# Optimization experiments

Hardware: AMD Instinct MI355X
Metric: run time of the kernel (lower is better)

## Reference

```python
import jax, jax.numpy as jnp
import numpy as np

D_MODEL = 512
D_ATTN = 512

def setup_inputs() -> dict:
    key = jax.random.key(0)
    kx, kq, kk, kv = jax.random.split(key, 4)
    x = jax.random.normal(kx, (8, 2048, D_MODEL), dtype=jnp.float32)
    s = 1.0 / np.sqrt(D_MODEL)
    Wq = jax.random.normal(kq, (D_ATTN, D_MODEL), dtype=jnp.float32) * s
    Wk = jax.random.normal(kk, (D_ATTN, D_MODEL), dtype=jnp.float32) * s
    Wv = jax.random.normal(kv, (D_MODEL, D_MODEL), dtype=jnp.float32) * s
    return {"x": x, "Wq": Wq, "Wk": Wk, "Wv": Wv}

def reference(x, Wq, Wk, Wv):
    # x: [B, S, D]; Linear(bias=False): y = x @ W.T
    q = jnp.einsum('bsd,ad->bsa', x, Wq)  # [B,S,Da]
    k = jnp.einsum('bsd,ad->bsa', x, Wk)  # [B,S,Da]
    v = jnp.einsum('bsd,ed->bse', x, Wv)  # [B,S,Dv]
    scale = 1.0 / jnp.sqrt(jnp.asarray(q.shape[-1], dtype=q.dtype))
    scores = jnp.einsum('bqa,bka->bqk', q, k) * scale  # [B,S,S]
    p = jax.nn.softmax(scores, axis=-1)
    return jnp.einsum('bqk,bke->bqe', p, v)
```

## Files before the change

kernel.cpp:

```cpp
#include <hip/hip_runtime.h>


typedef __bf16 bf16x8 __attribute__((ext_vector_type(8)));
typedef __bf16 bf16x4 __attribute__((ext_vector_type(4)));
typedef float  f32x4  __attribute__((ext_vector_type(4)));

constexpr int SEQ = 2048;
constexpr int DM  = 512;
constexpr int NB  = 8;
constexpr int GS  = NB * SEQ;
constexpr int NT2 = SEQ / 32;

__device__ __forceinline__ void gl16(const void* g, void* l) {
  __builtin_amdgcn_global_load_lds((const __attribute__((address_space(1))) void*)g,
                                   (__attribute__((address_space(3))) void*)l, 16, 0, 0);
}

__device__ __forceinline__ f32x4 mfma16(bf16x8 a, bf16x8 b, f32x4 c) {
  return __builtin_amdgcn_mfma_f32_16x16x32_bf16(a, b, c, 0, 0, 0);
}

__global__ void convert_kernel(const float* __restrict__ x,
                               const float* __restrict__ wq,
                               const float* __restrict__ wk,
                               const float* __restrict__ wv,
                               __bf16* __restrict__ xb,
                               __bf16* __restrict__ wqb,
                               __bf16* __restrict__ wkb,
                               __bf16* __restrict__ wvb) {
  const int NX4 = (GS * DM) / 4;
  const int NW4 = (DM * DM) / 4;
  const int stride = gridDim.x * blockDim.x;
  const int tid = blockIdx.x * blockDim.x + threadIdx.x;
  for (int i = tid; i < NX4; i += stride) {
    float4 v = ((const float4*)x)[i];
    bf16x4 o = { (__bf16)v.x, (__bf16)v.y, (__bf16)v.z, (__bf16)v.w };
    ((bf16x4*)xb)[i] = o;
  }
  for (int i = tid; i < NW4; i += stride) {
    float4 v = ((const float4*)wq)[i];
    bf16x4 o = { (__bf16)v.x, (__bf16)v.y, (__bf16)v.z, (__bf16)v.w };
    ((bf16x4*)wqb)[i] = o;
  }
  for (int i = tid; i < NW4; i += stride) {
    float4 v = ((const float4*)wk)[i];
    bf16x4 o = { (__bf16)v.x, (__bf16)v.y, (__bf16)v.z, (__bf16)v.w };
    ((bf16x4*)wkb)[i] = o;
  }
  for (int i = tid; i < NW4; i += stride) {
    float4 v = ((const float4*)wv)[i];
    bf16x4 o = { (__bf16)v.x, (__bf16)v.y, (__bf16)v.z, (__bf16)v.w };
    ((bf16x4*)wvb)[i] = o;
  }
}

__global__ __launch_bounds__(256, 2) void gemm_nt_kernel(
    const __bf16* __restrict__ A, const __bf16* __restrict__ Bm,
    __bf16* __restrict__ C, int N) {
  __shared__ __bf16 As[128 * 32];
  __shared__ __bf16 Bs[128 * 32];
  const int t = threadIdx.x;
  const int w = t >> 6, l = t & 63;
  const int l15 = l & 15, lg = l >> 4;
  const int m0 = blockIdx.x * 128, n0 = blockIdx.y * 128;
  const int wr = w >> 1, wc = w & 1;

  f32x4 acc[4][4] = {};
  const char* Ab = (const char*)A + (size_t)m0 * (DM * 2);
  const char* Bb = (const char*)Bm + (size_t)n0 * (DM * 2);

  for (int k0 = 0; k0 < DM; k0 += 32) {
#pragma unroll
    for (int i = 0; i < 2; ++i) {
      const int f = (i * 256 + t) * 16;
      const int row = f >> 6, c = f & 63;
      gl16(Ab + (size_t)row * (DM * 2) + k0 * 2 + c, (char*)As + f);
      gl16(Bb + (size_t)row * (DM * 2) + k0 * 2 + c, (char*)Bs + f);
    }
    __syncthreads();
    bf16x8 af[4], bfr[4];
#pragma unroll
    for (int mi = 0; mi < 4; ++mi)
      af[mi] = *(const bf16x8*)((const char*)As + (wr * 64 + mi * 16 + l15) * 64 + lg * 16);
#pragma unroll
    for (int ni = 0; ni < 4; ++ni)
      bfr[ni] = *(const bf16x8*)((const char*)Bs + (wc * 64 + ni * 16 + l15) * 64 + lg * 16);
#pragma unroll
    for (int mi = 0; mi < 4; ++mi)
#pragma unroll
      for (int ni = 0; ni < 4; ++ni)
        acc[mi][ni] = mfma16(af[mi], bfr[ni], acc[mi][ni]);
    __syncthreads();
  }
#pragma unroll
  for (int mi = 0; mi < 4; ++mi)
#pragma unroll
    for (int ni = 0; ni < 4; ++ni)
#pragma unroll
      for (int r = 0; r < 4; ++r) {
        const int row = m0 + wr * 64 + mi * 16 + lg * 4 + r;
        const int col = n0 + wc * 64 + ni * 16 + l15;
        C[(size_t)row * N + col] = (__bf16)acc[mi][ni][r];
      }
}

__global__ __launch_bounds__(256, 2) void attn_kernel(
    const __bf16* __restrict__ QK, const __bf16* __restrict__ Vt,
    float* __restrict__ Out) {
  __shared__ __bf16 Ks[32 * 512];
  __shared__ __bf16 Vs[512 * 32];
  __shared__ float  Ss[32 * 36];
  __shared__ __bf16 Ps[32 * 32];
  __shared__ float  m_s[32], l_s[32], corr_s[32];
  __shared__ int    flags_s[4];

  const int t = threadIdx.x;
  const int w = t >> 6, l = t & 63;
  const int l15 = l & 15, lg = l >> 4;
  const int bid = blockIdx.x;
  const int b = bid & 7;
  const int q0 = (bid >> 3) * 32;
  const int qi = w >> 1, kj = w & 1;

  bf16x8 qf[16];
  {
    const char* Qb = (const char*)QK +
        (size_t)(b * SEQ + q0 + qi * 16 + l15) * 2048 + lg * 16;
#pragma unroll
    for (int ks = 0; ks < 16; ++ks)
      qf[ks] = *(const bf16x8*)(Qb + ks * 64);
  }

  f32x4 o[2][8] = {};
  if (t < 32) { m_s[t] = -__builtin_inff(); l_s[t] = 0.f; }

  const char* Kb = (const char*)QK + (size_t)b * SEQ * 2048 + 1024;
  const char* Vb = (const char*)Vt + (size_t)b * SEQ * 2;

#pragma unroll
  for (int i = 0; i < 8; ++i) {
    const int f = (i * 256 + t) * 16;
    const int row = f >> 10, c = f & 1023;
    gl16(Kb + (size_t)row * 2048 + (c ^ ((row & 7) << 4)), (char*)Ks + f);
  }
  __syncthreads();

  const float SCL = 0.0637639022f;

  for (int it = 0; it < NT2; ++it) {
    const int kv0 = it * 32;

#pragma unroll
    for (int i = 0; i < 8; ++i) {
      const int f = (i * 256 + t) * 16;
      const int e = f >> 6, c2 = f & 63;
      gl16(Vb + (size_t)e * (GS * 2) + (size_t)kv0 * 2 + (c2 ^ ((e & 3) << 4)),
           (char*)Vs + f);
    }
    {
      f32x4 sa = {};
      const int krow = kj * 16 + l15;
      const char* KsR = (const char*)Ks + krow * 1024;
      const int ksw = (krow & 7) << 4;
#pragma unroll
      for (int ks = 0; ks < 16; ++ks) {
        bf16x8 kf = *(const bf16x8*)(KsR + ((ks * 64 + lg * 16) ^ ksw));
        sa = mfma16(qf[ks], kf, sa);
      }
#pragma unroll
      for (int r = 0; r < 4; ++r)
        Ss[(qi * 16 + lg * 4 + r) * 36 + kj * 16 + l15] = sa[r] * SCL;
    }
    __syncthreads();

    {
      const int row = t >> 3, c8 = t & 7;
      float4 v0 = *(const float4*)&Ss[row * 36 + c8 * 4];
      float tmax = fmaxf(fmaxf(v0.x, v0.y), fmaxf(v0.z, v0.w));
      tmax = fmaxf(tmax, __shfl_xor(tmax, 1));
      tmax = fmaxf(tmax, __shfl_xor(tmax, 2));
      tmax = fmaxf(tmax, __shfl_xor(tmax, 4));
      const float mold = m_s[row];
      const float mnew = fmaxf(mold, tmax);
      const float corr = exp2f(mold - mnew);
      const float p0 = exp2f(v0.x - mnew), p1 = exp2f(v0.y - mnew);
      const float p2 = exp2f(v0.z - mnew), p3 = exp2f(v0.w - mnew);
      float rsum = (p0 + p1) + (p2 + p3);
      rsum += __shfl_xor(rsum, 1);
      rsum += __shfl_xor(rsum, 2);
      rsum += __shfl_xor(rsum, 4);
      if (c8 == 0) { m_s[row] = mnew; l_s[row] = l_s[row] * corr + rsum; corr_s[row] = corr; }
      const int allskip = __all(corr == 1.0f);
      if (l == 0) flags_s[w] = allskip;
      bf16x4 pb = { (__bf16)p0, (__bf16)p1, (__bf16)p2, (__bf16)p3 };
      *(bf16x4*)((char*)Ps + row * 64 + (((c8 >> 1) * 16) ^ ((row & 3) << 4)) +
                 (c8 & 1) * 8) = pb;
    }
    __syncthreads();

    {
      const int kvn = ((it + 1) == NT2 ? 0 : (it + 1)) * 32;
#pragma unroll
      for (int i = 0; i < 8; ++i) {
        const int f = (i * 256 + t) * 16;
        const int row = f >> 10, c = f & 1023;
        gl16(Kb + (size_t)(kvn + row) * 2048 + (c ^ ((row & 7) << 4)), (char*)Ks + f);
      }
      const int fl = flags_s[0] & flags_s[1] & flags_s[2] & flags_s[3];
      if (!fl) {
#pragma unroll
        for (int mi = 0; mi < 2; ++mi) {
          float cr[4];
#pragma unroll
          for (int r = 0; r < 4; ++r) cr[r] = corr_s[mi * 16 + lg * 4 + r];
#pragma unroll
          for (int ni = 0; ni < 8; ++ni)
#pragma unroll
            for (int r = 0; r < 4; ++r) o[mi][ni][r] *= cr[r];
        }
      }
      bf16x8 pf[2];
#pragma unroll
      for (int mi = 0; mi < 2; ++mi) {
        const int prow = mi * 16 + l15;
        pf[mi] = *(const bf16x8*)((const char*)Ps + prow * 64 +
                                  ((lg * 16) ^ ((prow & 3) << 4)));
      }
#pragma unroll
      for (int ni = 0; ni < 8; ++ni) {
        const int er = w * 128 + ni * 16 + l15;
        bf16x8 vf = *(const bf16x8*)((const char*)Vs + er * 64 +
                                     ((lg * 16) ^ ((er & 3) << 4)));
#pragma unroll
        for (int mi = 0; mi < 2; ++mi)
          o[mi][ni] = mfma16(pf[mi], vf, o[mi][ni]);
      }
    }
    __syncthreads();
  }

#pragma unroll
  for (int mi = 0; mi < 2; ++mi) {
    float rl[4];
#pragma unroll
    for (int r = 0; r < 4; ++r) rl[r] = 1.0f / l_s[mi * 16 + lg * 4 + r];
#pragma unroll
    for (int ni = 0; ni < 8; ++ni)
#pragma unroll
      for (int r = 0; r < 4; ++r) {
        const int row = q0 + mi * 16 + lg * 4 + r;
        const int col = w * 128 + ni * 16 + l15;
        Out[((size_t)b * SEQ + row) * DM + col] = o[mi][ni][r] * rl[r];
      }
  }
}

extern "C" void kernel_launch(void* const* d_in, const int* in_sizes, int n_in,
                              void* d_out, int out_size, void* d_ws, size_t ws_size,
                              hipStream_t stream) {
  const float* x  = (const float*)d_in[0];
  const float* wq = (const float*)d_in[1];
  const float* wk = (const float*)d_in[2];
  const float* wv = (const float*)d_in[3];
  float* out = (float*)d_out;
  char* ws = (char*)d_ws;

  __bf16* xb   = (__bf16*)(ws);
  __bf16* wqkb = (__bf16*)(ws + 16777216);
  __bf16* wvb  = (__bf16*)(ws + 17825792);
  __bf16* qk   = (__bf16*)(ws + 18350080);
  __bf16* vt   = (__bf16*)(ws + 51904512);

  convert_kernel<<<2048, 256, 0, stream>>>(x, wq, wk, wv,
                                           xb, wqkb, wqkb + 262144, wvb);
  gemm_nt_kernel<<<dim3(GS / 128, 1024 / 128), 256, 0, stream>>>(xb, wqkb, qk, 1024);
  gemm_nt_kernel<<<dim3(DM / 128, GS / 128), 256, 0, stream>>>(wvb, xb, vt, GS);
  attn_kernel<<<512, 256, 0, stream>>>(qk, vt, out);
}
```

Baseline: 273.3 us.

## Double-buffer K/V tiles and widen attention blocks to 64 query rows

```diff
diff --git a/kernel.cpp b/kernel.cpp
--- a/kernel.cpp
+++ b/kernel.cpp
@@ -104,23 +104,36 @@
       }
 }
 
-__global__ __launch_bounds__(256, 2) void attn_kernel(
+__global__ __launch_bounds__(512, 2) void attn_kernel(
     const __bf16* __restrict__ QK, const __bf16* __restrict__ Vt,
     float* __restrict__ Out) {
-  __shared__ __bf16 Ks[32 * 512];
-  __shared__ __bf16 Vs[512 * 32];
-  __shared__ float  Ss[32 * 36];
-  __shared__ __bf16 Ps[32 * 32];
-  __shared__ float  m_s[32], l_s[32], corr_s[32];
-  __shared__ int    flags_s[4];
+  __shared__ __bf16 Ks[2][32 * 512];
+  __shared__ __bf16 Vs[2][512 * 32];
+  __shared__ float  Ss[64 * 36];
+  __shared__ __bf16 Ps[64 * 32];
+  __shared__ float  m_s[64], l_s[64], corr_s[64];
+  __shared__ int    flags_s[8];
 
   const int t = threadIdx.x;
   const int w = t >> 6, l = t & 63;
   const int l15 = l & 15, lg = l >> 4;
-  const int bid = blockIdx.x;
-  const int b = bid & 7;
-  const int q0 = (bid >> 3) * 32;
+  const int b = blockIdx.x & 7;
+  const int q0 = (blockIdx.x >> 3) * 64;
   const int qi = w >> 1, kj = w & 1;
+
+  int ksrc[4], vsrc[4], ldst[4];
+#pragma unroll
+  for (int i = 0; i < 4; ++i) {
+    const int f = (i * 512 + t) * 16;
+    ldst[i] = f;
+    const int krow = f >> 10, kc = f & 1023;
+    ksrc[i] = krow * 2048 + (kc ^ ((krow & 7) << 4));
+    const int e = f >> 6, c2 = f & 63;
+    vsrc[i] = e * (GS * 2) + (c2 ^ ((e & 3) << 4));
+  }
+
+  const char* Kb = (const char*)QK + (size_t)b * SEQ * 2048 + 1024;
+  const char* Vb = (const char*)Vt + (size_t)b * SEQ * 2;
 
   bf16x8 qf[16];
   {
@@ -131,47 +144,53 @@
       qf[ks] = *(const bf16x8*)(Qb + ks * 64);
   }
 
-  f32x4 o[2][8] = {};
-  if (t < 32) { m_s[t] = -__builtin_inff(); l_s[t] = 0.f; }
-
-  const char* Kb = (const char*)QK + (size_t)b * SEQ * 2048 + 1024;
-  const char* Vb = (const char*)Vt + (size_t)b * SEQ * 2;
-
-#pragma unroll
-  for (int i = 0; i < 8; ++i) {
-    const int f = (i * 256 + t) * 16;
-    const int row = f >> 10, c = f & 1023;
-    gl16(Kb + (size_t)row * 2048 + (c ^ ((row & 7) << 4)), (char*)Ks + f);
-  }
-  __syncthreads();
+  f32x4 o[4][4] = {};
+  if (t < 64) { m_s[t] = -__builtin_inff(); l_s[t] = 0.f; }
+
+#pragma unroll
+  for (int i = 0; i < 4; ++i) gl16(Kb + ksrc[i], (char*)&Ks[0][0] + ldst[i]);
+#pragma unroll
+  for (int i = 0; i < 4; ++i) gl16(Vb + vsrc[i], (char*)&Vs[0][0] + ldst[i]);
 
   const float SCL = 0.0637639022f;
 
   for (int it = 0; it < NT2; ++it) {
-    const int kv0 = it * 32;
-
-#pragma unroll
-    for (int i = 0; i < 8; ++i) {
-      const int f = (i * 256 + t) * 16;
-      const int e = f >> 6, c2 = f & 63;
-      gl16(Vb + (size_t)e * (GS * 2) + (size_t)kv0 * 2 + (c2 ^ ((e & 3) << 4)),
-           (char*)Vs + f);
-    }
-    {
-      f32x4 sa = {};
+    const int cur = it & 1;
+
+    asm volatile("s_waitcnt vmcnt(0) lgkmcnt(0)" ::: "memory");
+    __builtin_amdgcn_s_barrier();
+
+    {
+      const int kvn = (it + 1 < NT2 ? it + 1 : 0) * 32;
+      char* kdst = (char*)&Ks[cur ^ 1][0];
+      char* vdst = (char*)&Vs[cur ^ 1][0];
+#pragma unroll
+      for (int i = 0; i < 4; ++i) gl16(Kb + (size_t)kvn * 2048 + ksrc[i], kdst + ldst[i]);
+#pragma unroll
+      for (int i = 0; i < 4; ++i) gl16(Vb + (size_t)kvn * 2 + vsrc[i], vdst + ldst[i]);
+    }
+
+    {
+      f32x4 s0 = {}, s1 = {};
       const int krow = kj * 16 + l15;
-      const char* KsR = (const char*)Ks + krow * 1024;
+      const char* KsR = (const char*)&Ks[cur][0] + krow * 1024;
       const int ksw = (krow & 7) << 4;
-#pragma unroll
-      for (int ks = 0; ks < 16; ++ks) {
-        bf16x8 kf = *(const bf16x8*)(KsR + ((ks * 64 + lg * 16) ^ ksw));
-        sa = mfma16(qf[ks], kf, sa);
-      }
+      __builtin_amdgcn_s_setprio(1);
+#pragma unroll
+      for (int ks = 0; ks < 8; ++ks) {
+        bf16x8 kf0 = *(const bf16x8*)(KsR + ((ks * 64 + lg * 16) ^ ksw));
+        bf16x8 kf1 = *(const bf16x8*)(KsR + (((ks + 8) * 64 + lg * 16) ^ ksw));
+        s0 = mfma16(qf[ks], kf0, s0);
+        s1 = mfma16(qf[ks + 8], kf1, s1);
+      }
+      __builtin_amdgcn_s_setprio(0);
+      s0 = s0 + s1;
 #pragma unroll
       for (int r = 0; r < 4; ++r)
-        Ss[(qi * 16 + lg * 4 + r) * 36 + kj * 16 + l15] = sa[r] * SCL;
-    }
-    __syncthreads();
+        Ss[(qi * 16 + lg * 4 + r) * 36 + kj * 16 + l15] = s0[r] * SCL;
+    }
+    asm volatile("s_waitcnt lgkmcnt(0)" ::: "memory");
+    __builtin_amdgcn_s_barrier();
 
     {
       const int row = t >> 3, c8 = t & 7;
@@ -196,60 +215,57 @@
       *(bf16x4*)((char*)Ps + row * 64 + (((c8 >> 1) * 16) ^ ((row & 3) << 4)) +
                  (c8 & 1) * 8) = pb;
     }
-    __syncthreads();
-
-    {
-      const int kvn = ((it + 1) == NT2 ? 0 : (it + 1)) * 32;
-#pragma unroll
-      for (int i = 0; i < 8; ++i) {
-        const int f = (i * 256 + t) * 16;
-        const int row = f >> 10, c = f & 1023;
-        gl16(Kb + (size_t)(kvn + row) * 2048 + (c ^ ((row & 7) << 4)), (char*)Ks + f);
-      }
-      const int fl = flags_s[0] & flags_s[1] & flags_s[2] & flags_s[3];
+    asm volatile("s_waitcnt lgkmcnt(0)" ::: "memory");
+    __builtin_amdgcn_s_barrier();
+
+    {
+      int fl = 1;
+#pragma unroll
+      for (int i = 0; i < 8; ++i) fl &= flags_s[i];
       if (!fl) {
 #pragma unroll
-        for (int mi = 0; mi < 2; ++mi) {
+        for (int mi = 0; mi < 4; ++mi) {
           float cr[4];
 #pragma unroll
           for (int r = 0; r < 4; ++r) cr[r] = corr_s[mi * 16 + lg * 4 + r];
 #pragma unroll
-          for (int ni = 0; ni < 8; ++ni)
+          for (int ni = 0; ni < 4; ++ni)
 #pragma unroll
             for (int r = 0; r < 4; ++r) o[mi][ni][r] *= cr[r];
         }
       }
-      bf16x8 pf[2];
-#pragma unroll
-      for (int mi = 0; mi < 2; ++mi) {
+      bf16x8 pf[4];
+#pragma unroll
+      for (int mi = 0; mi < 4; ++mi) {
         const int prow = mi * 16 + l15;
         pf[mi] = *(const bf16x8*)((const char*)Ps + prow * 64 +
                                   ((lg * 16) ^ ((prow & 3) << 4)));
       }
-#pragma unroll
-      for (int ni = 0; ni < 8; ++ni) {
-        const int er = w * 128 + ni * 16 + l15;
-        bf16x8 vf = *(const bf16x8*)((const char*)Vs + er * 64 +
+      __builtin_amdgcn_s_setprio(1);
+#pragma unroll
+      for (int ni = 0; ni < 4; ++ni) {
+        const int er = w * 64 + ni * 16 + l15;
+        bf16x8 vf = *(const bf16x8*)((const char*)&Vs[cur][0] + er * 64 +
                                      ((lg * 16) ^ ((er & 3) << 4)));
 #pragma unroll
-        for (int mi = 0; mi < 2; ++mi)
+        for (int mi = 0; mi < 4; ++mi)
           o[mi][ni] = mfma16(pf[mi], vf, o[mi][ni]);
       }
-    }
-    __syncthreads();
-  }
-
-#pragma unroll
-  for (int mi = 0; mi < 2; ++mi) {
+      __builtin_amdgcn_s_setprio(0);
+    }
+  }
+
+#pragma unroll
+  for (int mi = 0; mi < 4; ++mi) {
     float rl[4];
 #pragma unroll
     for (int r = 0; r < 4; ++r) rl[r] = 1.0f / l_s[mi * 16 + lg * 4 + r];
 #pragma unroll
-    for (int ni = 0; ni < 8; ++ni)
+    for (int ni = 0; ni < 4; ++ni)
 #pragma unroll
       for (int r = 0; r < 4; ++r) {
         const int row = q0 + mi * 16 + lg * 4 + r;
-        const int col = w * 128 + ni * 16 + l15;
+        const int col = w * 64 + ni * 16 + l15;
         Out[((size_t)b * SEQ + row) * DM + col] = o[mi][ni][r] * rl[r];
       }
   }
@@ -275,5 +291,5 @@
                                            xb, wqkb, wqkb + 262144, wvb);
   gemm_nt_kernel<<<dim3(GS / 128, 1024 / 128), 256, 0, stream>>>(xb, wqkb, qk, 1024);
   gemm_nt_kernel<<<dim3(DM / 128, GS / 128), 256, 0, stream>>>(wvb, xb, vt, GS);
-  attn_kernel<<<512, 256, 0, stream>>>(qk, vt, out);
-}
+  attn_kernel<<<256, 512, 0, stream>>>(qk, vt, out);
+}
```

New measurement: 289.6 us. +6.0%, slower.

## Split attention QK^T across 8 waves with LDS atomic reduction and fold scale into Wq

Applied to the files above, without the earlier changes.

```diff
diff --git a/kernel.cpp b/kernel.cpp
--- a/kernel.cpp
+++ b/kernel.cpp
@@ -30,6 +30,7 @@
                                __bf16* __restrict__ wvb) {
   const int NX4 = (GS * DM) / 4;
   const int NW4 = (DM * DM) / 4;
+  const float SCL = 0.0637639022f;
   const int stride = gridDim.x * blockDim.x;
   const int tid = blockIdx.x * blockDim.x + threadIdx.x;
   for (int i = tid; i < NX4; i += stride) {
@@ -39,7 +40,8 @@
   }
   for (int i = tid; i < NW4; i += stride) {
     float4 v = ((const float4*)wq)[i];
-    bf16x4 o = { (__bf16)v.x, (__bf16)v.y, (__bf16)v.z, (__bf16)v.w };
+    bf16x4 o = { (__bf16)(v.x * SCL), (__bf16)(v.y * SCL),
+                 (__bf16)(v.z * SCL), (__bf16)(v.w * SCL) };
     ((bf16x4*)wqb)[i] = o;
   }
   for (int i = tid; i < NW4; i += stride) {
@@ -104,109 +106,123 @@
       }
 }
 
-__global__ __launch_bounds__(256, 2) void attn_kernel(
+__global__ __launch_bounds__(512, 4) void attn_kernel(
     const __bf16* __restrict__ QK, const __bf16* __restrict__ Vt,
     float* __restrict__ Out) {
-  __shared__ __bf16 Ks[32 * 512];
-  __shared__ __bf16 Vs[512 * 32];
-  __shared__ float  Ss[32 * 36];
+  __shared__ __align__(16) __bf16 Ks[32 * 512];
+  __shared__ __align__(16) __bf16 Vs[512 * 32];
+  __shared__ float  Sa[32 * 34];
   __shared__ __bf16 Ps[32 * 32];
   __shared__ float  m_s[32], l_s[32], corr_s[32];
-  __shared__ int    flags_s[4];
+  __shared__ int    flags_s[8];
 
   const int t = threadIdx.x;
   const int w = t >> 6, l = t & 63;
   const int l15 = l & 15, lg = l >> 4;
-  const int bid = blockIdx.x;
-  const int b = bid & 7;
-  const int q0 = (bid >> 3) * 32;
-  const int qi = w >> 1, kj = w & 1;
-
-  bf16x8 qf[16];
-  {
-    const char* Qb = (const char*)QK +
-        (size_t)(b * SEQ + q0 + qi * 16 + l15) * 2048 + lg * 16;
-#pragma unroll
-    for (int ks = 0; ks < 16; ++ks)
-      qf[ks] = *(const bf16x8*)(Qb + ks * 64);
-  }
-
-  f32x4 o[2][8] = {};
-  if (t < 32) { m_s[t] = -__builtin_inff(); l_s[t] = 0.f; }
-
+  const int b = blockIdx.x & 7;
+  const int q0 = (blockIdx.x >> 3) * 32;
+  const int dh = w & 3;
+  const int kj = w >> 2;
+
+  char* KsB = (char*)Ks;
+  char* VsB = (char*)Vs;
   const char* Kb = (const char*)QK + (size_t)b * SEQ * 2048 + 1024;
   const char* Vb = (const char*)Vt + (size_t)b * SEQ * 2;
 
-#pragma unroll
-  for (int i = 0; i < 8; ++i) {
-    const int f = (i * 256 + t) * 16;
-    const int row = f >> 10, c = f & 1023;
-    gl16(Kb + (size_t)row * 2048 + (c ^ ((row & 7) << 4)), (char*)Ks + f);
-  }
+  const int krow_sw = (w & 7) << 4;
+  const int ksrc0 = w * 2048 + ((l * 16) ^ krow_sw);
+  const int ve = t >> 2;
+  const int vsrc0 = (((t & 3) << 4) ^ ((ve & 3) << 4));
+  const int vdst0 = ve * 64 + ((t & 3) << 4);
+
+  bf16x8 qf[2][4];
+  {
+    const char* Qp = (const char*)QK + (size_t)(b * SEQ + q0 + l15) * 2048 +
+                     dh * 256 + lg * 16;
+#pragma unroll
+    for (int mi = 0; mi < 2; ++mi)
+#pragma unroll
+      for (int ks = 0; ks < 4; ++ks)
+        qf[mi][ks] = *(const bf16x8*)(Qp + (size_t)mi * 16 * 2048 + ks * 64);
+  }
+
+  f32x4 o[2][4] = {};
+
+  for (int idx = t; idx < 32 * 34; idx += 512) Sa[idx] = 0.f;
+  if (t < 32) { m_s[t] = -__builtin_inff(); l_s[t] = 0.f; }
+#pragma unroll
+  for (int i = 0; i < 4; ++i)
+    gl16(Kb + i * 8 * 2048 + ksrc0, KsB + (i * 512 + t) * 16);
   __syncthreads();
 
-  const float SCL = 0.0637639022f;
-
   for (int it = 0; it < NT2; ++it) {
-    const int kv0 = it * 32;
-
-#pragma unroll
-    for (int i = 0; i < 8; ++i) {
-      const int f = (i * 256 + t) * 16;
-      const int e = f >> 6, c2 = f & 63;
-      gl16(Vb + (size_t)e * (GS * 2) + (size_t)kv0 * 2 + (c2 ^ ((e & 3) << 4)),
-           (char*)Vs + f);
-    }
+    const size_t kv0 = (size_t)it * 32;
+
+#pragma unroll
+    for (int i = 0; i < 4; ++i)
+      gl16(Vb + kv0 * 2 + (size_t)(i * 128 + ve) * (GS * 2) + vsrc0,
+           VsB + i * 8192 + vdst0);
     {
-      f32x4 sa = {};
-      const int krow = kj * 16 + l15;
-      const char* KsR = (const char*)Ks + krow * 1024;
-      const int ksw = (krow & 7) << 4;
-#pragma unroll
-      for (int ks = 0; ks < 16; ++ks) {
-        bf16x8 kf = *(const bf16x8*)(KsR + ((ks * 64 + lg * 16) ^ ksw));
-        sa = mfma16(qf[ks], kf, sa);
-      }
-#pragma unroll
-      for (int r = 0; r < 4; ++r)
-        Ss[(qi * 16 + lg * 4 + r) * 36 + kj * 16 + l15] = sa[r] * SCL;
+      f32x4 s0 = {}, s1 = {};
+      const char* KsR = KsB + (kj * 16 + l15) * 1024;
+      const int ksw = (l15 & 7) << 4;
+      __builtin_amdgcn_s_setprio(1);
+#pragma unroll
+      for (int ks = 0; ks < 4; ++ks) {
+        bf16x8 kf = *(const bf16x8*)(KsR + ((dh * 256 + ks * 64 + lg * 16) ^ ksw));
+        s0 = mfma16(qf[0][ks], kf, s0);
+        s1 = mfma16(qf[1][ks], kf, s1);
+      }
+      __builtin_amdgcn_s_setprio(0);
+      const int scol = kj * 16 + l15;
+#pragma unroll
+      for (int r = 0; r < 4; ++r) {
+        atomicAdd(&Sa[(lg * 4 + r) * 34 + scol], s0[r]);
+        atomicAdd(&Sa[(16 + lg * 4 + r) * 34 + scol], s1[r]);
+      }
     }
     __syncthreads();
 
     {
-      const int row = t >> 3, c8 = t & 7;
-      float4 v0 = *(const float4*)&Ss[row * 36 + c8 * 4];
-      float tmax = fmaxf(fmaxf(v0.x, v0.y), fmaxf(v0.z, v0.w));
+      const int row = t >> 4, c = t & 15;
+      float a0 = Sa[row * 34 + 2 * c];
+      float a1 = Sa[row * 34 + 2 * c + 1];
+      Sa[row * 34 + 2 * c] = 0.f;
+      Sa[row * 34 + 2 * c + 1] = 0.f;
+      float tmax = fmaxf(a0, a1);
       tmax = fmaxf(tmax, __shfl_xor(tmax, 1));
       tmax = fmaxf(tmax, __shfl_xor(tmax, 2));
       tmax = fmaxf(tmax, __shfl_xor(tmax, 4));
+      tmax = fmaxf(tmax, __shfl_xor(tmax, 8));
       const float mold = m_s[row];
       const float mnew = fmaxf(mold, tmax);
       const float corr = exp2f(mold - mnew);
-      const float p0 = exp2f(v0.x - mnew), p1 = exp2f(v0.y - mnew);
-      const float p2 = exp2f(v0.z - mnew), p3 = exp2f(v0.w - mnew);
-      float rsum = (p0 + p1) + (p2 + p3);
+      const float p0 = exp2f(a0 - mnew), p1 = exp2f(a1 - mnew);
+      float rsum = p0 + p1;
       rsum += __shfl_xor(rsum, 1);
       rsum += __shfl_xor(rsum, 2);
       rsum += __shfl_xor(rsum, 4);
-      if (c8 == 0) { m_s[row] = mnew; l_s[row] = l_s[row] * corr + rsum; corr_s[row] = corr; }
+      rsum += __shfl_xor(rsum, 8);
+      if (c == 0) { m_s[row] = mnew; l_s[row] = l_s[row] * corr + rsum; corr_s[row] = corr; }
       const int allskip = __all(corr == 1.0f);
       if (l == 0) flags_s[w] = allskip;
-      bf16x4 pb = { (__bf16)p0, (__bf16)p1, (__bf16)p2, (__bf16)p3 };
-      *(bf16x4*)((char*)Ps + row * 64 + (((c8 >> 1) * 16) ^ ((row & 3) << 4)) +
-                 (c8 & 1) * 8) = pb;
+      unsigned short u0 = __builtin_bit_cast(unsigned short, (__bf16)p0);
+      unsigned short u1 = __builtin_bit_cast(unsigned short, (__bf16)p1);
+      unsigned int pp = (unsigned int)u0 | ((unsigned int)u1 << 16);
+      *(unsigned int*)((char*)Ps + row * 64 + (((c >> 2) ^ (row & 3)) << 4) +
+                       (c & 3) * 4) = pp;
     }
     __syncthreads();
 
     {
-      const int kvn = ((it + 1) == NT2 ? 0 : (it + 1)) * 32;
-#pragma unroll
-      for (int i = 0; i < 8; ++i) {
-        const int f = (i * 256 + t) * 16;
-        const int row = f >> 10, c = f & 1023;
-        gl16(Kb + (size_t)(kvn + row) * 2048 + (c ^ ((row & 7) << 4)), (char*)Ks + f);
-      }
-      const int fl = flags_s[0] & flags_s[1] & flags_s[2] & flags_s[3];
+      const size_t kvn = (size_t)((it + 1) & (NT2 - 1)) * 32;
+#pragma unroll
+      for (int i = 0; i < 4; ++i)
+        gl16(Kb + (kvn + i * 8) * 2048 + ksrc0, KsB + (i * 512 + t) * 16);
+
+      int fl = 1;
+#pragma unroll
+      for (int i = 0; i < 8; ++i) fl &= flags_s[i];
       if (!fl) {
 #pragma unroll
         for (int mi = 0; mi < 2; ++mi) {
@@ -214,7 +230,7 @@
 #pragma unroll
           for (int r = 0; r < 4; ++r) cr[r] = corr_s[mi * 16 + lg * 4 + r];
 #pragma unroll
-          for (int ni = 0; ni < 8; ++ni)
+          for (int ni = 0; ni < 4; ++ni)
 #pragma unroll
             for (int r = 0; r < 4; ++r) o[mi][ni][r] *= cr[r];
         }
@@ -224,17 +240,19 @@
       for (int mi = 0; mi < 2; ++mi) {
         const int prow = mi * 16 + l15;
         pf[mi] = *(const bf16x8*)((const char*)Ps + prow * 64 +
-                                  ((lg * 16) ^ ((prow & 3) << 4)));
-      }
-#pragma unroll
-      for (int ni = 0; ni < 8; ++ni) {
-        const int er = w * 128 + ni * 16 + l15;
+                                  ((lg ^ (prow & 3)) << 4));
+      }
+      __builtin_amdgcn_s_setprio(1);
+#pragma unroll
+      for (int ni = 0; ni < 4; ++ni) {
+        const int er = w * 64 + ni * 16 + l15;
         bf16x8 vf = *(const bf16x8*)((const char*)Vs + er * 64 +
-                                     ((lg * 16) ^ ((er & 3) << 4)));
+                                     ((lg ^ (er & 3)) << 4));
 #pragma unroll
         for (int mi = 0; mi < 2; ++mi)
           o[mi][ni] = mfma16(pf[mi], vf, o[mi][ni]);
       }
+      __builtin_amdgcn_s_setprio(0);
     }
     __syncthreads();
   }
@@ -245,11 +263,11 @@
 #pragma unroll
     for (int r = 0; r < 4; ++r) rl[r] = 1.0f / l_s[mi * 16 + lg * 4 + r];
 #pragma unroll
-    for (int ni = 0; ni < 8; ++ni)
+    for (int ni = 0; ni < 4; ++ni)
 #pragma unroll
       for (int r = 0; r < 4; ++r) {
         const int row = q0 + mi * 16 + lg * 4 + r;
-        const int col = w * 128 + ni * 16 + l15;
+        const int col = w * 64 + ni * 16 + l15;
         Out[((size_t)b * SEQ + row) * DM + col] = o[mi][ni][r] * rl[r];
       }
   }
@@ -275,5 +293,5 @@
                                            xb, wqkb, wqkb + 262144, wvb);
   gemm_nt_kernel<<<dim3(GS / 128, 1024 / 128), 256, 0, stream>>>(xb, wqkb, qk, 1024);
   gemm_nt_kernel<<<dim3(DM / 128, GS / 128), 256, 0, stream>>>(wvb, xb, vt, GS);
-  attn_kernel<<<512, 256, 0, stream>>>(qk, vt, out);
-}
+  attn_kernel<<<512, 512, 0, stream>>>(qk, vt, out);
+}
```

Result: slower. 926.7 us (+239.1%).

## Double attention KV tile to 64 and stream V fragments straight from global

Applied to the files above, without the earlier changes.

```diff
diff --git a/kernel.cpp b/kernel.cpp
--- a/kernel.cpp
+++ b/kernel.cpp
@@ -9,7 +9,7 @@
 constexpr int DM  = 512;
 constexpr int NB  = 8;
 constexpr int GS  = NB * SEQ;
-constexpr int NT2 = SEQ / 32;
+constexpr int NT  = SEQ / 64;
 
 __device__ __forceinline__ void gl16(const void* g, void* l) {
   __builtin_amdgcn_global_load_lds((const __attribute__((address_space(1))) void*)g,
@@ -30,6 +30,7 @@
                                __bf16* __restrict__ wvb) {
   const int NX4 = (GS * DM) / 4;
   const int NW4 = (DM * DM) / 4;
+  const float SCL = 0.0637639022f;
   const int stride = gridDim.x * blockDim.x;
   const int tid = blockIdx.x * blockDim.x + threadIdx.x;
   for (int i = tid; i < NX4; i += stride) {
@@ -39,7 +40,8 @@
   }
   for (int i = tid; i < NW4; i += stride) {
     float4 v = ((const float4*)wq)[i];
-    bf16x4 o = { (__bf16)v.x, (__bf16)v.y, (__bf16)v.z, (__bf16)v.w };
+    bf16x4 o = { (__bf16)(v.x * SCL), (__bf16)(v.y * SCL),
+                 (__bf16)(v.z * SCL), (__bf16)(v.w * SCL) };
     ((bf16x4*)wqb)[i] = o;
   }
   for (int i = tid; i < NW4; i += stride) {
@@ -107,76 +109,92 @@
 __global__ __launch_bounds__(256, 2) void attn_kernel(
     const __bf16* __restrict__ QK, const __bf16* __restrict__ Vt,
     float* __restrict__ Out) {
-  __shared__ __bf16 Ks[32 * 512];
-  __shared__ __bf16 Vs[512 * 32];
-  __shared__ float  Ss[32 * 36];
-  __shared__ __bf16 Ps[32 * 32];
+  __shared__ __align__(16) __bf16 Ks[64 * 512];
+  __shared__ float  Ss[32 * 68];
+  __shared__ __align__(16) __bf16 Ps[32 * 64];
   __shared__ float  m_s[32], l_s[32], corr_s[32];
   __shared__ int    flags_s[4];
 
   const int t = threadIdx.x;
   const int w = t >> 6, l = t & 63;
   const int l15 = l & 15, lg = l >> 4;
-  const int bid = blockIdx.x;
-  const int b = bid & 7;
-  const int q0 = (bid >> 3) * 32;
+  const int b = blockIdx.x & 7;
+  const int q0 = (blockIdx.x >> 3) * 32;
   const int qi = w >> 1, kj = w & 1;
+
+  char* KsB = (char*)Ks;
+  const char* Kb = (const char*)QK + (size_t)b * SEQ * 2048 + 1024;
+  const char* Vb = (const char*)Vt + (size_t)b * SEQ * 2;
 
   bf16x8 qf[16];
   {
-    const char* Qb = (const char*)QK +
-        (size_t)(b * SEQ + q0 + qi * 16 + l15) * 2048 + lg * 16;
+    const char* Qp = (const char*)QK + (size_t)(b * SEQ + q0 + qi * 16 + l15) * 2048 + lg * 16;
 #pragma unroll
     for (int ks = 0; ks < 16; ++ks)
-      qf[ks] = *(const bf16x8*)(Qb + ks * 64);
+      qf[ks] = *(const bf16x8*)(Qp + ks * 64);
   }
 
   f32x4 o[2][8] = {};
   if (t < 32) { m_s[t] = -__builtin_inff(); l_s[t] = 0.f; }
 
-  const char* Kb = (const char*)QK + (size_t)b * SEQ * 2048 + 1024;
-  const char* Vb = (const char*)Vt + (size_t)b * SEQ * 2;
-
-#pragma unroll
-  for (int i = 0; i < 8; ++i) {
+#pragma unroll
+  for (int i = 0; i < 16; ++i) {
     const int f = (i * 256 + t) * 16;
     const int row = f >> 10, c = f & 1023;
-    gl16(Kb + (size_t)row * 2048 + (c ^ ((row & 7) << 4)), (char*)Ks + f);
+    gl16(Kb + (size_t)row * 2048 + (c ^ ((row & 7) << 4)), KsB + f);
   }
   __syncthreads();
 
-  const float SCL = 0.0637639022f;
-
-  for (int it = 0; it < NT2; ++it) {
-    const int kv0 = it * 32;
-
-#pragma unroll
-    for (int i = 0; i < 8; ++i) {
-      const int f = (i * 256 + t) * 16;
-      const int e = f >> 6, c2 = f & 63;
-      gl16(Vb + (size_t)e * (GS * 2) + (size_t)kv0 * 2 + (c2 ^ ((e & 3) << 4)),
-           (char*)Vs + f);
+  const int kswz = (l15 & 7) << 4;
+  const char* KsR0 = KsB + (kj * 32 + l15) * 1024;
+  const char* KsR1 = KsR0 + 16 * 1024;
+  const size_t vstep = (size_t)GS * 2;
+
+  for (int it = 0; it < NT; ++it) {
+    const size_t kv0 = (size_t)it * 64;
+
+    bf16x8 vfA[4][2];
+#pragma unroll
+    for (int ni = 0; ni < 4; ++ni)
+#pragma unroll
+      for (int ks = 0; ks < 2; ++ks)
+        vfA[ni][ks] = *(const bf16x8*)(Vb + (size_t)(w * 128 + ni * 16 + l15) * vstep +
+                                       (kv0 + ks * 32 + lg * 8) * 2);
+    {
+      f32x4 s0 = {}, s1 = {};
+      __builtin_amdgcn_s_setprio(1);
+#pragma unroll
+      for (int ks = 0; ks < 16; ++ks) {
+        const int c = (ks * 64 + lg * 16) ^ kswz;
+        bf16x8 kf0 = *(const bf16x8*)(KsR0 + c);
+        bf16x8 kf1 = *(const bf16x8*)(KsR1 + c);
+        s0 = mfma16(qf[ks], kf0, s0);
+        s1 = mfma16(qf[ks], kf1, s1);
+      }
+      __builtin_amdgcn_s_setprio(0);
+#pragma unroll
+      for (int r = 0; r < 4; ++r) {
+        Ss[(qi * 16 + lg * 4 + r) * 68 + kj * 32 + l15] = s0[r];
+        Ss[(qi * 16 + lg * 4 + r) * 68 + kj * 32 + 16 + l15] = s1[r];
+      }
     }
+    asm volatile("s_waitcnt lgkmcnt(0)" ::: "memory");
+    __builtin_amdgcn_s_barrier();
+
     {
-      f32x4 sa = {};
-      const int krow = kj * 16 + l15;
-      const char* KsR = (const char*)Ks + krow * 1024;
-      const int ksw = (krow & 7) << 4;
-#pragma unroll
-      for (int ks = 0; ks < 16; ++ks) {
-        bf16x8 kf = *(const bf16x8*)(KsR + ((ks * 64 + lg * 16) ^ ksw));
-        sa = mfma16(qf[ks], kf, sa);
-      }
-#pragma unroll
-      for (int r = 0; r < 4; ++r)
-        Ss[(qi * 16 + lg * 4 + r) * 36 + kj * 16 + l15] = sa[r] * SCL;
-    }
-    __syncthreads();
-
-    {
+      const size_t kvn = (size_t)((it + 1) & (NT - 1)) * 64;
+#pragma unroll
+      for (int i = 0; i < 16; ++i) {
+        const int f = (i * 256 + t) * 16;
+        const int row = f >> 10, c = f & 1023;
+        gl16(Kb + (kvn + row) * 2048 + (c ^ ((row & 7) << 4)), KsB + f);
+      }
       const int row = t >> 3, c8 = t & 7;
-      float4 v0 = *(const float4*)&Ss[row * 36 + c8 * 4];
-      float tmax = fmaxf(fmaxf(v0.x, v0.y), fmaxf(v0.z, v0.w));
+      const float* Sr = &Ss[row * 68 + c8 * 8];
+      float4 v0 = *(const float4*)(Sr);
+      float4 v1 = *(const float4*)(Sr + 4);
+      float tmax = fmaxf(fmaxf(fmaxf(v0.x, v0.y), fmaxf(v0.z, v0.w)),
+                         fmaxf(fmaxf(v1.x, v1.y), fmaxf(v1.z, v1.w)));
       tmax = fmaxf(tmax, __shfl_xor(tmax, 1));
       tmax = fmaxf(tmax, __shfl_xor(tmax, 2));
       tmax = fmaxf(tmax, __shfl_xor(tmax, 4));
@@ -185,27 +203,23 @@
       const float corr = exp2f(mold - mnew);
       const float p0 = exp2f(v0.x - mnew), p1 = exp2f(v0.y - mnew);
       const float p2 = exp2f(v0.z - mnew), p3 = exp2f(v0.w - mnew);
-      float rsum = (p0 + p1) + (p2 + p3);
+      const float p4 = exp2f(v1.x - mnew), p5 = exp2f(v1.y - mnew);
+      const float p6 = exp2f(v1.z - mnew), p7 = exp2f(v1.w - mnew);
+      float rsum = ((p0 + p1) + (p2 + p3)) + ((p4 + p5) + (p6 + p7));
       rsum += __shfl_xor(rsum, 1);
       rsum += __shfl_xor(rsum, 2);
       rsum += __shfl_xor(rsum, 4);
       if (c8 == 0) { m_s[row] = mnew; l_s[row] = l_s[row] * corr + rsum; corr_s[row] = corr; }
       const int allskip = __all(corr == 1.0f);
       if (l == 0) flags_s[w] = allskip;
-      bf16x4 pb = { (__bf16)p0, (__bf16)p1, (__bf16)p2, (__bf16)p3 };
-      *(bf16x4*)((char*)Ps + row * 64 + (((c8 >> 1) * 16) ^ ((row & 3) << 4)) +
-                 (c8 & 1) * 8) = pb;
+      bf16x8 pb = { (__bf16)p0, (__bf16)p1, (__bf16)p2, (__bf16)p3,
+                    (__bf16)p4, (__bf16)p5, (__bf16)p6, (__bf16)p7 };
+      *(bf16x8*)((char*)Ps + row * 128 + ((c8 * 16) ^ ((row & 7) << 4))) = pb;
     }
-    __syncthreads();
+    asm volatile("s_waitcnt lgkmcnt(0)" ::: "memory");
+    __builtin_amdgcn_s_barrier();
 
     {
-      const int kvn = ((it + 1) == NT2 ? 0 : (it + 1)) * 32;
-#pragma unroll
-      for (int i = 0; i < 8; ++i) {
-        const int f = (i * 256 + t) * 16;
-        const int row = f >> 10, c = f & 1023;
-        gl16(Kb + (size_t)(kvn + row) * 2048 + (c ^ ((row & 7) << 4)), (char*)Ks + f);
-      }
       const int fl = flags_s[0] & flags_s[1] & flags_s[2] & flags_s[3];
       if (!fl) {
 #pragma unroll
@@ -219,24 +233,41 @@
             for (int r = 0; r < 4; ++r) o[mi][ni][r] *= cr[r];
         }
       }
-      bf16x8 pf[2];
-#pragma unroll
-      for (int mi = 0; mi < 2; ++mi) {
-        const int prow = mi * 16 + l15;
-        pf[mi] = *(const bf16x8*)((const char*)Ps + prow * 64 +
-                                  ((lg * 16) ^ ((prow & 3) << 4)));
-      }
-#pragma unroll
-      for (int ni = 0; ni < 8; ++ni) {
-        const int er = w * 128 + ni * 16 + l15;
-        bf16x8 vf = *(const bf16x8*)((const char*)Vs + er * 64 +
-                                     ((lg * 16) ^ ((er & 3) << 4)));
-#pragma unroll
-        for (int mi = 0; mi < 2; ++mi)
-          o[mi][ni] = mfma16(pf[mi], vf, o[mi][ni]);
-      }
+      bf16x8 pf[2][2];
+#pragma unroll
+      for (int mi = 0; mi < 2; ++mi)
+#pragma unroll
+        for (int ks = 0; ks < 2; ++ks)
+          pf[mi][ks] = *(const bf16x8*)((const char*)Ps + (mi * 16 + l15) * 128 +
+                                        ((ks * 64 + lg * 16) ^ kswz));
+      __builtin_amdgcn_s_setprio(1);
+#pragma unroll
+      for (int ks = 0; ks < 2; ++ks)
+#pragma unroll
+        for (int ni = 0; ni < 4; ++ni)
+#pragma unroll
+          for (int mi = 0; mi < 2; ++mi)
+            o[mi][ni] = mfma16(pf[mi][ks], vfA[ni][ks], o[mi][ni]);
+      __builtin_amdgcn_s_setprio(0);
+      bf16x8 vfB[4][2];
+#pragma unroll
+      for (int ni = 0; ni < 4; ++ni)
+#pragma unroll
+        for (int ks = 0; ks < 2; ++ks)
+          vfB[ni][ks] = *(const bf16x8*)(Vb + (size_t)(w * 128 + 64 + ni * 16 + l15) * vstep +
+                                         (kv0 + ks * 32 + lg * 8) * 2);
+      __builtin_amdgcn_s_setprio(1);
+#pragma unroll
+      for (int ks = 0; ks < 2; ++ks)
+#pragma unroll
+        for (int ni = 0; ni < 4; ++ni)
+#pragma unroll
+          for (int mi = 0; mi < 2; ++mi)
+            o[mi][ni + 4] = mfma16(pf[mi][ks], vfB[ni][ks], o[mi][ni + 4]);
+      __builtin_amdgcn_s_setprio(0);
     }
-    __syncthreads();
+    asm volatile("s_waitcnt vmcnt(0) lgkmcnt(0)" ::: "memory");
+    __builtin_amdgcn_s_barrier();
   }
 
 #pragma unroll
```

After: 325.3 us. 1.19x slower.
